# Performance work log

Hardware: AMD Instinct MI355X
Metric: run time of the kernel (lower is better)

Reference implementation:

```python
import jax, jax.numpy as jnp
import numpy as np

B, D, H, O = 16384, 256, 64, 256


def setup_inputs() -> dict:
    key = jax.random.key(0)
    ks = jax.random.split(key, 7)
    s1 = 1.0  # Linear(1,H): fan_in=1 -> U(-1,1)
    sH = 1.0 / np.sqrt(H)
    sD = 1.0 / np.sqrt(D)
    return {
        "x": jax.random.normal(ks[0], (B, D), dtype=jnp.float32),
        "W1": jax.random.uniform(ks[1], (D, H), jnp.float32, -s1, s1),
        "b1": jax.random.uniform(ks[2], (D, H), jnp.float32, -s1, s1),
        "W2": jax.random.uniform(ks[3], (D, H), jnp.float32, -sH, sH),
        "b2": jax.random.uniform(ks[4], (D,), jnp.float32, -sH, sH),
        "Wc": jax.random.uniform(ks[5], (O, D), jnp.float32, -sD, sD),
        "bc": jax.random.uniform(ks[6], (O,), jnp.float32, -sD, sD),
    }


def reference(x, W1, b1, W2, b2, Wc, bc):
    # Per-feature tiny MLP, batched over the feature axis D.
    # hidden: [B, D, H]
    h = jax.nn.relu(x[:, :, None] * W1[None, :, :] + b1[None, :, :])
    # collapse hidden -> scalar per feature: [B, D]
    u = jnp.einsum("bdh,dh->bd", h, W2) + b2[None, :]
    # combiner Linear(D, O)
    return u @ Wc.T + bc[None, :]
```

## Files before the change

kernel.cpp:

```cpp
#include <hip/hip_runtime.h>
#include <hip/hip_bf16.h>
#include <hip/hip_fp16.h>

#define B_N 16384
#define D_N 256
#define H_N 64
#define O_N 256

typedef unsigned int u32;
typedef unsigned short u16;
typedef _Float16 f16;
typedef __attribute__((ext_vector_type(2))) _Float16 f16x2;
typedef __attribute__((ext_vector_type(8))) _Float16 f16x8;
typedef __attribute__((ext_vector_type(4))) float f32x4;
typedef __attribute__((ext_vector_type(4))) u32 uint4v;
typedef __attribute__((ext_vector_type(4))) u16 u16x4;

__device__ uint4v g_W1p[8 * 256];
__device__ uint4v g_B1p[8 * 256];
__device__ uint4v g_W2p[8 * 256];
__device__ __attribute__((aligned(16))) u16 g_Wch[O_N * D_N];

union HU { f16 h; u16 b; };

static __device__ __forceinline__ u32 packh2(float a, float b) {
  f16x2 p = {(f16)a, (f16)b};
  return __builtin_bit_cast(u32, p);
}
static __device__ __forceinline__ u16 f16b(float a) {
  HU u; u.h = (f16)a; return u.b;
}
static __device__ __forceinline__ f16x2 ash2(u32 w) {
  return __builtin_bit_cast(f16x2, w);
}

#if __has_builtin(__builtin_amdgcn_fdot2)
#define FDOT2(a, b, c) __builtin_amdgcn_fdot2((a), (b), (c), false)
#else
#define FDOT2(a, b, c) \
  fmaf((float)(a)[0], (float)(b)[0], fmaf((float)(a)[1], (float)(b)[1], (c)))
#endif

__global__ __launch_bounds__(256) void prep(
    const float* __restrict__ W1, const float* __restrict__ b1,
    const float* __restrict__ W2, const float* __restrict__ Wc) {
  const int u = blockIdx.x * 256 + threadIdx.x;
  const int d = u >> 6, h = u & 63;
  if ((h & 1) == 0) {
    const int j = h >> 1;
    const int idx = ((j >> 2) * 256 + d) * 4 + (j & 3);
    ((u32*)g_W1p)[idx] = packh2(W1[u], W1[u + 1]);
    ((u32*)g_B1p)[idx] = packh2(b1[u], b1[u + 1]);
    ((u32*)g_W2p)[idx] = packh2(W2[u], W2[u + 1]);
  }
  const int i4 = u * 4;
  const f32x4 v = *reinterpret_cast<const f32x4*>(Wc + i4);
  u16x4 s;
#pragma unroll
  for (int q = 0; q < 4; ++q) s[q] = f16b(v[q]);
  *reinterpret_cast<u16x4*>(g_Wch + i4) = s;
}

__global__ __launch_bounds__(256, 3) void kan_fused(
    const float* __restrict__ x, const float* __restrict__ b2,
    const float* __restrict__ bc, float* __restrict__ out) {
  __shared__ u16 uT[16 * 256];

  const int t  = threadIdx.x;
  const int b0 = blockIdx.x * 16;

  uint4v w1r[8], b1r[8], w2r[8];
#pragma unroll
  for (int i = 0; i < 8; ++i) {
    w1r[i] = g_W1p[i * 256 + t];
    b1r[i] = g_B1p[i * 256 + t];
    w2r[i] = g_W2p[i * 256 + t];
  }
  const float b2v = b2[t];

#pragma unroll
  for (int g = 0; g < 2; ++g) {
    f16x2 xx[8];
    float acc[8];
#pragma unroll
    for (int r = 0; r < 8; ++r) {
      const float xv = x[(b0 + g * 8 + r) * D_N + t];
      xx[r] = (f16x2){(f16)xv, (f16)xv};
      acc[r] = 0.f;
    }
#pragma unroll
    for (int i = 0; i < 8; ++i) {
#pragma unroll
      for (int q = 0; q < 4; ++q) {
        const f16x2 w1 = ash2(w1r[i][q]);
        const f16x2 bb = ash2(b1r[i][q]);
        const f16x2 w2 = ash2(w2r[i][q]);
#pragma unroll
        for (int r = 0; r < 8; ++r) {
          f16x2 tv = __builtin_elementwise_fma(xx[r], w1, bb);
          tv = __builtin_elementwise_max(tv, (f16x2){(f16)0.f, (f16)0.f});
          acc[r] = FDOT2(tv, w2, acc[r]);
        }
      }
    }
#pragma unroll
    for (int r = 0; r < 8; ++r) {
      const int row = g * 8 + r;
      int byte = row * 512 + t * 2;
      byte ^= (row & 7) << 4;
      *(u16*)((char*)uT + byte) = f16b(acc[r] + b2v);
    }
  }
  __syncthreads();

  const int wv   = t >> 6;
  const int dl   = t & 63;
  const int n0   = wv * 64;
  const int mrow = dl & 15;
  const int kgrp = dl >> 4;

  f32x4 acc2[4];
#pragma unroll
  for (int j = 0; j < 4; ++j) acc2[j] = (f32x4)(0.f);

#pragma unroll
  for (int ks = 0; ks < 8; ++ks) {
    const int k0 = ks * 32 + kgrp * 8;
    int byte = mrow * 512 + k0 * 2;
    byte ^= (mrow & 7) << 4;
    const f16x8 afrag = *reinterpret_cast<const f16x8*>((const char*)uT + byte);
#pragma unroll
    for (int j = 0; j < 4; ++j) {
      const f16x8 bfrag = *reinterpret_cast<const f16x8*>(
          g_Wch + (n0 + j * 16 + mrow) * D_N + k0);
      acc2[j] = __builtin_amdgcn_mfma_f32_16x16x32_f16(afrag, bfrag, acc2[j],
                                                       0, 0, 0);
    }
  }

#pragma unroll
  for (int j = 0; j < 4; ++j) {
    const int colg = n0 + j * 16 + mrow;
    const float bcv = bc[colg];
#pragma unroll
    for (int q = 0; q < 4; ++q) {
      const int rowg = b0 + kgrp * 4 + q;
      out[rowg * O_N + colg] = acc2[j][q] + bcv;
    }
  }
}

extern "C" void kernel_launch(void* const* d_in, const int* in_sizes, int n_in,
                              void* d_out, int out_size, void* d_ws, size_t ws_size,
                              hipStream_t stream) {
  const float* x  = (const float*)d_in[0];
  const float* W1 = (const float*)d_in[1];
  const float* b1 = (const float*)d_in[2];
  const float* W2 = (const float*)d_in[3];
  const float* b2 = (const float*)d_in[4];
  const float* Wc = (const float*)d_in[5];
  const float* bc = (const float*)d_in[6];
  float* out = (float*)d_out;

  prep<<<dim3(D_N * H_N / 256), dim3(256), 0, stream>>>(W1, b1, W2, Wc);
  kan_fused<<<dim3(B_N / 16), dim3(256), 0, stream>>>(x, b2, bc, out);
}
```

Baseline: 103.7 us.

## Split fused kernel into per-feature MLP pass and MFMA combiner pass

The fused kernel is replaced by two kernels. The first maps threads to batch rows over a 16-feature slice, so weights are read from wave-uniform addresses (scalar/broadcast loads) instead of being held in 96 VGPRs per thread. It writes u as fp16 to a global buffer laid out in MFMA fragment order. The second kernel runs the 16x16x32 MFMA combiner directly from that buffer. This frees register pressure and raises occupancy, at the cost of an extra global round-trip for u (about 8 MB) and one more kernel launch.

```diff
diff --git a/kernel.cpp b/kernel.cpp
--- a/kernel.cpp
+++ b/kernel.cpp
@@ -1,5 +1,4 @@
 #include <hip/hip_runtime.h>
-#include <hip/hip_bf16.h>
 #include <hip/hip_fp16.h>
 
 #define B_N 16384
@@ -16,10 +15,11 @@
 typedef __attribute__((ext_vector_type(4))) u32 uint4v;
 typedef __attribute__((ext_vector_type(4))) u16 u16x4;
 
-__device__ uint4v g_W1p[8 * 256];
-__device__ uint4v g_B1p[8 * 256];
-__device__ uint4v g_W2p[8 * 256];
+__device__ u32 g_Wp [D_N * 32];
+__device__ u32 g_Bp [D_N * 32];
+__device__ u32 g_W2p[D_N * 32];
 __device__ __attribute__((aligned(16))) u16 g_Wch[O_N * D_N];
+__device__ __attribute__((aligned(16))) u16 g_Uf[B_N * D_N];
 
 union HU { f16 h; u16 b; };
 
@@ -27,12 +27,8 @@
   f16x2 p = {(f16)a, (f16)b};
   return __builtin_bit_cast(u32, p);
 }
-static __device__ __forceinline__ u16 f16b(float a) {
-  HU u; u.h = (f16)a; return u.b;
-}
-static __device__ __forceinline__ f16x2 ash2(u32 w) {
-  return __builtin_bit_cast(f16x2, w);
-}
+static __device__ __forceinline__ u16 f16b(float a) { HU u; u.h = (f16)a; return u.b; }
+static __device__ __forceinline__ f16x2 ash2(u32 w) { return __builtin_bit_cast(f16x2, w); }
 
 #if __has_builtin(__builtin_amdgcn_fdot2)
 #define FDOT2(a, b, c) __builtin_amdgcn_fdot2((a), (b), (c), false)
@@ -44,16 +40,15 @@
 __global__ __launch_bounds__(256) void prep(
     const float* __restrict__ W1, const float* __restrict__ b1,
     const float* __restrict__ W2, const float* __restrict__ Wc) {
-  const int u = blockIdx.x * 256 + threadIdx.x;
-  const int d = u >> 6, h = u & 63;
-  if ((h & 1) == 0) {
-    const int j = h >> 1;
-    const int idx = ((j >> 2) * 256 + d) * 4 + (j & 3);
-    ((u32*)g_W1p)[idx] = packh2(W1[u], W1[u + 1]);
-    ((u32*)g_B1p)[idx] = packh2(b1[u], b1[u + 1]);
-    ((u32*)g_W2p)[idx] = packh2(W2[u], W2[u + 1]);
+  const int t = blockIdx.x * 256 + threadIdx.x;
+  if ((t & 1) == 0) {
+    const int d = t >> 6, j = (t & 63) >> 1;
+    const int idx = d * 32 + j;
+    g_Wp[idx]  = packh2(W1[t], W1[t + 1]);
+    g_Bp[idx]  = packh2(b1[t], b1[t + 1]);
+    g_W2p[idx] = packh2(W2[t], W2[t + 1]);
   }
-  const int i4 = u * 4;
+  const int i4 = t * 4;
   const f32x4 v = *reinterpret_cast<const f32x4*>(Wc + i4);
   u16x4 s;
 #pragma unroll
@@ -61,63 +56,59 @@
   *reinterpret_cast<u16x4*>(g_Wch + i4) = s;
 }
 
-__global__ __launch_bounds__(256, 3) void kan_fused(
-    const float* __restrict__ x, const float* __restrict__ b2,
-    const float* __restrict__ bc, float* __restrict__ out) {
-  __shared__ u16 uT[16 * 256];
+__global__ __launch_bounds__(256) void kan_p1(const float* __restrict__ x,
+                                              const float* __restrict__ b2) {
+  const int tid = threadIdx.x;
+  const int b   = (blockIdx.x >> 4) * 256 + tid;
+  const int d0  = (blockIdx.x & 15) * 16;
 
-  const int t  = threadIdx.x;
-  const int b0 = blockIdx.x * 16;
+  f32x4 xr[4];
+#pragma unroll
+  for (int c = 0; c < 4; ++c)
+    xr[c] = *reinterpret_cast<const f32x4*>(x + b * D_N + d0 + c * 4);
 
-  uint4v w1r[8], b1r[8], w2r[8];
+  float uo[16];
 #pragma unroll
-  for (int i = 0; i < 8; ++i) {
-    w1r[i] = g_W1p[i * 256 + t];
-    b1r[i] = g_B1p[i * 256 + t];
-    w2r[i] = g_W2p[i * 256 + t];
-  }
-  const float b2v = b2[t];
-
+  for (int c = 0; c < 4; ++c) {
 #pragma unroll
-  for (int g = 0; g < 2; ++g) {
-    f16x2 xx[8];
-    float acc[8];
+    for (int e = 0; e < 4; ++e) {
+      const int dd = c * 4 + e;
+      const int d  = d0 + dd;
+      const f16 hx = (f16)xr[c][e];
+      const f16x2 xx = {hx, hx};
+      float acc = 0.f;
+      const u32* __restrict__ wp  = g_Wp  + d * 32;
+      const u32* __restrict__ bp  = g_Bp  + d * 32;
+      const u32* __restrict__ w2p = g_W2p + d * 32;
 #pragma unroll
-    for (int r = 0; r < 8; ++r) {
-      const float xv = x[(b0 + g * 8 + r) * D_N + t];
-      xx[r] = (f16x2){(f16)xv, (f16)xv};
-      acc[r] = 0.f;
-    }
-#pragma unroll
-    for (int i = 0; i < 8; ++i) {
-#pragma unroll
-      for (int q = 0; q < 4; ++q) {
-        const f16x2 w1 = ash2(w1r[i][q]);
-        const f16x2 bb = ash2(b1r[i][q]);
-        const f16x2 w2 = ash2(w2r[i][q]);
-#pragma unroll
-        for (int r = 0; r < 8; ++r) {
-          f16x2 tv = __builtin_elementwise_fma(xx[r], w1, bb);
-          tv = __builtin_elementwise_max(tv, (f16x2){(f16)0.f, (f16)0.f});
-          acc[r] = FDOT2(tv, w2, acc[r]);
-        }
+      for (int j = 0; j < 32; ++j) {
+        f16x2 tv = __builtin_elementwise_fma(xx, ash2(wp[j]), ash2(bp[j]));
+        tv = __builtin_elementwise_max(tv, (f16x2){(f16)0.f, (f16)0.f});
+        acc = FDOT2(tv, ash2(w2p[j]), acc);
       }
-    }
-#pragma unroll
-    for (int r = 0; r < 8; ++r) {
-      const int row = g * 8 + r;
-      int byte = row * 512 + t * 2;
-      byte ^= (row & 7) << 4;
-      *(u16*)((char*)uT + byte) = f16b(acc[r] + b2v);
+      uo[dd] = acc + b2[d];
     }
   }
-  __syncthreads();
 
-  const int wv   = t >> 6;
-  const int dl   = t & 63;
+  const int base = ((b >> 4) * 32 + (d0 >> 3)) * 128 + (b & 15) * 8;
+#pragma unroll
+  for (int half = 0; half < 2; ++half) {
+    union { u16 h[8]; uint4v v; } pk;
+#pragma unroll
+    for (int e = 0; e < 8; ++e) pk.h[e] = f16b(uo[half * 8 + e]);
+    *reinterpret_cast<uint4v*>(g_Uf + base + half * 128) = pk.v;
+  }
+}
+
+__global__ __launch_bounds__(256) void kan_p2(const float* __restrict__ bc,
+                                              float* __restrict__ out) {
+  const int t    = threadIdx.x;
+  const int wv   = t >> 6, dl = t & 63;
+  const int mt   = blockIdx.x;
   const int n0   = wv * 64;
   const int mrow = dl & 15;
   const int kgrp = dl >> 4;
+  const int b0   = mt * 16;
 
   f32x4 acc2[4];
 #pragma unroll
@@ -126,9 +117,8 @@
 #pragma unroll
   for (int ks = 0; ks < 8; ++ks) {
     const int k0 = ks * 32 + kgrp * 8;
-    int byte = mrow * 512 + k0 * 2;
-    byte ^= (mrow & 7) << 4;
-    const f16x8 afrag = *reinterpret_cast<const f16x8*>((const char*)uT + byte);
+    const f16x8 afrag = *reinterpret_cast<const f16x8*>(
+        g_Uf + (mt * 32 + ks * 4 + kgrp) * 128 + mrow * 8);
 #pragma unroll
     for (int j = 0; j < 4; ++j) {
       const f16x8 bfrag = *reinterpret_cast<const f16x8*>(
@@ -163,5 +153,6 @@
   float* out = (float*)d_out;
 
   prep<<<dim3(D_N * H_N / 256), dim3(256), 0, stream>>>(W1, b1, W2, Wc);
-  kan_fused<<<dim3(B_N / 16), dim3(256), 0, stream>>>(x, b2, bc, out);
+  kan_p1<<<dim3((B_N / 256) * (D_N / 16)), dim3(256), 0, stream>>>(x, b2);
+  kan_p2<<<dim3(B_N / 16), dim3(256), 0, stream>>>(bc, out);
 }
```

Result: slower. 118.4 us (+14.2%).
